# Kernel optimization log

Hardware: AMD Instinct MI355X
Metric: run time of the kernel (lower is better)

Reference implementation:

```python
import jax, jax.numpy as jnp
import numpy as np

B, T, TR, D, H = 8, 1024, 256, 1024, 16
HS = D // H  # head size = 64
FF = 4 * D


def _ln(x, g, b, eps=1e-5):
    m = jnp.mean(x, axis=-1, keepdims=True)
    v = jnp.mean((x - m) ** 2, axis=-1, keepdims=True)
    return (x - m) * jax.lax.rsqrt(v + eps) * g + b


def setup_inputs() -> dict:
    key = jax.random.key(0)
    ks = jax.random.split(key, 24)
    w = lambda i, shape: jax.random.normal(ks[i], shape, dtype=jnp.float32) * 0.02
    return {
        "x": jax.random.normal(ks[0], (B, T, D), dtype=jnp.float32),
        # reduced positional embedding table (gathered by arange == table itself)
        "pos_emb": w(1, (TR, D)),
        # inner standard Block params
        "blk_ln1_g": jnp.ones((D,), jnp.float32), "blk_ln1_b": jnp.zeros((D,), jnp.float32),
        "blk_wq": w(2, (H, D, HS)), "blk_wk": w(3, (H, D, HS)), "blk_wv": w(4, (H, D, HS)),
        "blk_wo": w(5, (D, D)), "blk_bo": jnp.zeros((D,), jnp.float32),
        "blk_ln2_g": jnp.ones((D,), jnp.float32), "blk_ln2_b": jnp.zeros((D,), jnp.float32),
        "blk_w1": w(6, (D, FF)), "blk_b1": jnp.zeros((FF,), jnp.float32),
        "blk_w2": w(7, (FF, D)), "blk_b2": jnp.zeros((D,), jnp.float32),
        # compressing cross-attention params
        "ln1_g": jnp.ones((D,), jnp.float32), "ln1_b": jnp.zeros((D,), jnp.float32),
        "ca_wq": w(8, (H, D, HS)), "ca_wk": w(9, (H, D, HS)), "ca_wv": w(10, (H, D, HS)),
        "ca_wo": w(11, (D, D)), "ca_bo": jnp.zeros((D,), jnp.float32),
        "ln2_g": jnp.ones((D,), jnp.float32), "ln2_b": jnp.zeros((D,), jnp.float32),
        "ff_w1": w(12, (D, FF)), "ff_b1": jnp.zeros((FF,), jnp.float32),
        "ff_w2": w(13, (FF, D)), "ff_b2": jnp.zeros((D,), jnp.float32),
    }


def reference(x, pos_emb, blk_ln1_g, blk_ln1_b, blk_wq, blk_wk, blk_wv, blk_wo, blk_bo,
              blk_ln2_g, blk_ln2_b, blk_w1, blk_b1, blk_w2, blk_b2,
              ln1_g, ln1_b, ca_wq, ca_wk, ca_wv, ca_wo, ca_bo,
              ln2_g, ln2_b, ff_w1, ff_b1, ff_w2, ff_b2):
    b, t, c = x.shape
    scale = c ** -0.5  # matches q @ k^T * c**-0.5 in source

    # ---- inner standard Block: y = x + sa(ln1(x)); y = y + ffwd(ln2(y)) ----
    h = _ln(x, blk_ln1_g, blk_ln1_b)
    q = jnp.einsum('btc,hcs->bhts', h, blk_wq)
    k = jnp.einsum('btc,hcs->bhts', h, blk_wk)
    v = jnp.einsum('btc,hcs->bhts', h, blk_wv)
    wei = jnp.einsum('bhts,bhus->bhtu', q, k) * scale
    causal = jnp.tril(jnp.ones((t, t), dtype=bool))
    wei = jax.nn.softmax(jnp.where(causal, wei, -jnp.inf), axis=-1)
    att = jnp.einsum('bhtu,bhus->bhts', wei, v)
    att = att.transpose(0, 2, 1, 3).reshape(b, t, c) @ blk_wo + blk_bo
    y = x + att
    h2 = _ln(y, blk_ln2_g, blk_ln2_b)
    y = y + (jax.nn.relu(h2 @ blk_w1 + blk_b1) @ blk_w2 + blk_b2)

    # outer residual in CompressingBlock.forward
    x = x + y

    # ---- compressing cross-attention: queries/values from x, keys from pos emb ----
    h1 = _ln(x, ln1_g, ln1_b)
    q = jnp.einsum('btc,hcs->bhts', h1, ca_wq)
    kk = jnp.einsum('rc,hcs->hrs', pos_emb, ca_wk)  # same for every batch
    v = jnp.einsum('btc,hcs->bhts', h1, ca_wv)
    wei = jnp.einsum('bhts,hrs->bhtr', q, kk) * scale  # [b,h,t,tr]
    tr = pos_emb.shape[0]
    mask = jnp.tril(jnp.ones((t, tr), dtype=bool))  # tril[:t,:tr]
    wei = jax.nn.softmax(jnp.where(mask, wei, -jnp.inf), axis=-1)
    # transpose then wei^T @ v -> compressed sequence length tr
    out = jnp.einsum('bhtr,bhts->bhrs', wei, v)
    out = out.transpose(0, 2, 1, 3).reshape(b, tr, c) @ ca_wo + ca_bo

    # ---- final FFN with residual ----
    h3 = _ln(out, ln2_g, ln2_b)
    out = out + (jax.nn.relu(h3 @ ff_w1 + ff_b1) @ ff_w2 + ff_b2)
    return out
```

## Files before the change

kernel.cpp:

```cpp
#include <hip/hip_runtime.h>
#include <stdint.h>

typedef unsigned short u16;
typedef __attribute__((ext_vector_type(8))) short short8;
typedef __attribute__((ext_vector_type(4))) float f32x4;

#define MFMA16(A,B,C) __builtin_amdgcn_mfma_f32_16x16x32_bf16(A,B,C,0,0,0)

static __device__ __forceinline__ u16 f2bf(float f) {
  union { float f; unsigned u; } v; v.f = f;
  unsigned r = v.u + 0x7FFFu + ((v.u >> 16) & 1u);
  return (u16)(r >> 16);
}

static __device__ __forceinline__ void gload16(const void* g, void* l) {
  __builtin_amdgcn_global_load_lds(
      (const __attribute__((address_space(1))) void*)(uintptr_t)g,
      (__attribute__((address_space(3))) void*)(uint32_t)(uintptr_t)l,
      16, 0, 0);
}

static __device__ __forceinline__ int xcd_swz() {
  const int gx = gridDim.x, gy = gridDim.y, nwg = gx * gy;
  const int orig = blockIdx.y * gx + blockIdx.x;
  const int q = nwg >> 3, rm = nwg & 7, xcd = orig & 7, idx = orig >> 3;
  return (xcd < rm ? xcd * (q + 1) : rm * (q + 1) + (xcd - rm) * q) + idx;
}

#define GPH(CUR, STAGE_STMT, TAIL_STMT) do { \
  short8 af_[4], bf_[4]; \
  _Pragma("unroll") \
  for (int mf = 0; mf < 4; ++mf) { \
    const int r = wm0 + mf * 16 + colL; \
    af_[mf] = *(const short8*)&lds[(CUR) + r * 32 + ((kgr ^ ((r >> 1) & 3)) << 3)]; \
  } \
  _Pragma("unroll") \
  for (int nf = 0; nf < 4; ++nf) { \
    const int r = wn0 + nf * 16 + colL; \
    bf_[nf] = *(const short8*)&lds[(CUR) + 4096 + r * 32 + ((kgr ^ ((r >> 1) & 3)) << 3)]; \
  } \
  STAGE_STMT; \
  _Pragma("unroll") \
  for (int mf = 0; mf < 4; ++mf) \
    _Pragma("unroll") \
    for (int nf = 0; nf < 4; ++nf) \
      acc[mf][nf] = MFMA16(af_[mf], bf_[nf], acc[mf][nf]); \
  TAIL_STMT; \
  __builtin_amdgcn_sched_barrier(0); \
  __builtin_amdgcn_s_barrier(); \
  asm volatile("" ::: "memory"); \
} while (0)

__global__ __launch_bounds__(256) void gemm128p(
    const u16* __restrict__ A, const u16* __restrict__ Wt,
    float* __restrict__ Cf, u16* __restrict__ Cb,
    const float* __restrict__ bias,
    const float* __restrict__ res1, const float* __restrict__ res2,
    int M, int N, int K, int relu)
{
  __shared__ u16 lds[24576];
  const int tid = threadIdx.x;
  const int wid = tid >> 6, lane = tid & 63;
  const int colL = lane & 15, kgr = lane >> 4;
  const int wm0 = (wid & 1) * 64, wn0 = (wid >> 1) * 64;
  const int w = xcd_swz();
  const int m0 = (w / gridDim.y) * 128, n0 = (w % gridDim.y) * 128;
  const int U = K >> 5;
  f32x4 acc[4][4] = {};

  auto stageP = [&](int u, int bufo) {
    const int kb = u * 32;
#pragma unroll
    for (int i = 0; i < 2; ++i) {
      const int c = i * 256 + tid;
      const int row = c >> 2, slot = c & 3;
      const int cs = kb + ((slot ^ ((row >> 1) & 3)) << 3);
      gload16(A  + (size_t)(m0 + row) * K + cs,
              &lds[bufo + ((i * 256 + wid * 64) << 3)]);
      gload16(Wt + (size_t)(n0 + row) * K + cs,
              &lds[bufo + 4096 + ((i * 256 + wid * 64) << 3)]);
    }
  };

  int c0 = 0, c1 = 8192, c2 = 16384;
  stageP(0, c0); stageP(1, c1);
  asm volatile("s_waitcnt vmcnt(4)" ::: "memory");
  __builtin_amdgcn_s_barrier();
  asm volatile("" ::: "memory");

  for (int u = 0; u < U; ++u) {
    GPH(c0,
        { if (u + 2 < U) stageP(u + 2, c2); },
        { if (u + 2 < U) { asm volatile("s_waitcnt vmcnt(4)" ::: "memory"); }
          else           { asm volatile("s_waitcnt vmcnt(0)" ::: "memory"); } });
    const int tmp = c0; c0 = c1; c1 = c2; c2 = tmp;
  }

#pragma unroll
  for (int mf = 0; mf < 4; ++mf) {
#pragma unroll
    for (int nf = 0; nf < 4; ++nf) {
      const int n = n0 + wn0 + nf * 16 + colL;
      const float bv = bias ? bias[n] : 0.f;
#pragma unroll
      for (int rr = 0; rr < 4; ++rr) {
        const int m = m0 + wm0 + mf * 16 + kgr * 4 + rr;
        const size_t off = (size_t)m * N + n;
        float v = acc[mf][nf][rr] + bv;
        if (res1) v += res1[off];
        if (res2) v += res2[off];
        if (relu) v = fmaxf(v, 0.f);
        if (Cf) Cf[off] = v; else Cb[off] = f2bf(v);
      }
    }
  }
}

__global__ __launch_bounds__(256) void gemm128ks(
    const u16* __restrict__ A, const u16* __restrict__ Wt,
    float* __restrict__ Pf, int lda, int N, int K)
{
  __shared__ u16 lds[24576];
  const int tid = threadIdx.x;
  const int wid = tid >> 6, lane = tid & 63;
  const int colL = lane & 15, kgr = lane >> 4;
  const int wm0 = (wid & 1) * 64, wn0 = (wid >> 1) * 64;
  const int w = xcd_swz();
  const int m0 = (w / gridDim.y) * 128, n0 = (w % gridDim.y) * 128;
  const int koff = blockIdx.z * K;
  const int U = K >> 5;
  f32x4 acc[4][4] = {};

  auto stageP = [&](int u, int bufo) {
    const int kb = koff + u * 32;
#pragma unroll
    for (int i = 0; i < 2; ++i) {
      const int c = i * 256 + tid;
      const int row = c >> 2, slot = c & 3;
      const int cs = kb + ((slot ^ ((row >> 1) & 3)) << 3);
      gload16(A  + (size_t)(m0 + row) * lda + cs,
              &lds[bufo + ((i * 256 + wid * 64) << 3)]);
      gload16(Wt + (size_t)(n0 + row) * lda + cs,
              &lds[bufo + 4096 + ((i * 256 + wid * 64) << 3)]);
    }
  };

  int c0 = 0, c1 = 8192, c2 = 16384;
  stageP(0, c0); stageP(1, c1);
  asm volatile("s_waitcnt vmcnt(4)" ::: "memory");
  __builtin_amdgcn_s_barrier();
  asm volatile("" ::: "memory");

  for (int u = 0; u < U; ++u) {
    GPH(c0,
        { if (u + 2 < U) stageP(u + 2, c2); },
        { if (u + 2 < U) { asm volatile("s_waitcnt vmcnt(4)" ::: "memory"); }
          else           { asm volatile("s_waitcnt vmcnt(0)" ::: "memory"); } });
    const int tmp = c0; c0 = c1; c1 = c2; c2 = tmp;
  }

  float* out = Pf + (size_t)blockIdx.z * gridDim.x * 128 * N;
#pragma unroll
  for (int mf = 0; mf < 4; ++mf)
#pragma unroll
    for (int nf = 0; nf < 4; ++nf) {
      const int n = n0 + wn0 + nf * 16 + colL;
#pragma unroll
      for (int rr = 0; rr < 4; ++rr) {
        const int m = m0 + wm0 + mf * 16 + kgr * 4 + rr;
        out[(size_t)m * N + n] = acc[mf][nf][rr];
      }
    }
}

__global__ __launch_bounds__(256) void ffn2_reduce(
    const float* __restrict__ pf, const float* __restrict__ bias,
    const float* __restrict__ res, float* __restrict__ out)
{
  const size_t i = ((size_t)blockIdx.x * 256 + threadIdx.x) * 4;
  const size_t STRIDE = (size_t)2048 * 1024;
  const int col = (int)(i & 1023);
  float4 a = *(const float4*)(pf + i);
  const float4 b = *(const float4*)(pf + STRIDE + i);
  const float4 c = *(const float4*)(pf + 2 * STRIDE + i);
  const float4 d = *(const float4*)(pf + 3 * STRIDE + i);
  const float4 bv = *(const float4*)(bias + col);
  const float4 rv = *(const float4*)(res + i);
  float4 o;
  o.x = a.x + b.x + c.x + d.x + bv.x + rv.x;
  o.y = a.y + b.y + c.y + d.y + bv.y + rv.y;
  o.z = a.z + b.z + c.z + d.z + bv.z + rv.z;
  o.w = a.w + b.w + c.w + d.w + bv.w + rv.w;
  *(float4*)(out + i) = o;
}

__global__ __launch_bounds__(256) void ln_rows(
    const float* __restrict__ x, const float* __restrict__ g,
    const float* __restrict__ bt, u16* __restrict__ out)
{
  const int row = blockIdx.x, tid = threadIdx.x;
  const float4 v = ((const float4*)(x + (size_t)row * 1024))[tid];
  float s  = v.x + v.y + v.z + v.w;
  float ss = v.x * v.x + v.y * v.y + v.z * v.z + v.w * v.w;
#pragma unroll
  for (int off = 32; off; off >>= 1) {
    s  += __shfl_xor(s, off);
    ss += __shfl_xor(ss, off);
  }
  __shared__ float red[8];
  const int wid = tid >> 6, lane = tid & 63;
  if (lane == 0) { red[wid] = s; red[4 + wid] = ss; }
  __syncthreads();
  s  = red[0] + red[1] + red[2] + red[3];
  ss = red[4] + red[5] + red[6] + red[7];
  const float mean = s * 0.0009765625f;
  const float var  = ss * 0.0009765625f - mean * mean;
  const float rstd = rsqrtf(var + 1e-5f);
  const float4 gg = ((const float4*)g)[tid];
  const float4 bb = ((const float4*)bt)[tid];
  uint2 ov;
  ov.x = (unsigned)f2bf((v.x - mean) * rstd * gg.x + bb.x) |
         ((unsigned)f2bf((v.y - mean) * rstd * gg.y + bb.y) << 16);
  ov.y = (unsigned)f2bf((v.z - mean) * rstd * gg.z + bb.z) |
         ((unsigned)f2bf((v.w - mean) * rstd * gg.w + bb.w) << 16);
  *(uint2*)(out + (size_t)row * 1024 + tid * 4) = ov;
}

__global__ __launch_bounds__(256) void transpose_w(
    const float* __restrict__ in, u16* __restrict__ out, int R, int C)
{
  __shared__ float t[32][33];
  const int c0 = blockIdx.x * 32, r0 = blockIdx.y * 32;
  const int tx = threadIdx.x & 31, ty = threadIdx.x >> 5;
#pragma unroll
  for (int i = 0; i < 32; i += 8)
    t[ty + i][tx] = in[(size_t)(r0 + ty + i) * C + c0 + tx];
  __syncthreads();
#pragma unroll
  for (int i = 0; i < 32; i += 8)
    out[(size_t)(c0 + ty + i) * R + r0 + tx] = f2bf(t[tx][ty + i]);
}

__global__ __launch_bounds__(256) void pack_head_w(
    const float* __restrict__ w, u16* __restrict__ out)
{
  __shared__ float t[32][33];
  const int h = blockIdx.z;
  const int s0 = blockIdx.x * 32, c0 = blockIdx.y * 32;
  const int tx = threadIdx.x & 31, ty = threadIdx.x >> 5;
#pragma unroll
  for (int i = 0; i < 32; i += 8)
    t[ty + i][tx] = w[((size_t)h * 1024 + c0 + ty + i) * 64 + s0 + tx];
  __syncthreads();
#pragma unroll
  for (int i = 0; i < 32; i += 8)
    out[((size_t)h * 64 + s0 + ty + i) * 1024 + c0 + tx] = f2bf(t[tx][ty + i]);
}

__global__ __launch_bounds__(256) void cvt_bf16(
    const float* __restrict__ in, u16* __restrict__ out)
{
  const int i = blockIdx.x * blockDim.x + threadIdx.x;
  const float4 v = ((const float4*)in)[i];
  uint2 ov;
  ov.x = (unsigned)f2bf(v.x) | ((unsigned)f2bf(v.y) << 16);
  ov.y = (unsigned)f2bf(v.z) | ((unsigned)f2bf(v.w) << 16);
  *(uint2*)(out + (size_t)i * 4) = ov;
}

__global__ __launch_bounds__(256) void vtrans(
    const u16* __restrict__ src, u16* __restrict__ dst, int coloff, int ld)
{
  __shared__ u16 tile[64][65];
  const int t0 = blockIdx.x * 64, h = blockIdx.y, b = blockIdx.z;
  const int lr = threadIdx.x >> 4;
  const int lc = (threadIdx.x & 15) * 4;
#pragma unroll
  for (int i = 0; i < 64; i += 16) {
    const u16* sp = src + (size_t)(b * 1024 + t0 + lr + i) * ld + coloff + h * 64 + lc;
    const uint2 v = *(const uint2*)sp;
    tile[lr + i][lc + 0] = (u16)(v.x & 0xffff);
    tile[lr + i][lc + 1] = (u16)(v.x >> 16);
    tile[lr + i][lc + 2] = (u16)(v.y & 0xffff);
    tile[lr + i][lc + 3] = (u16)(v.y >> 16);
  }
  __syncthreads();
#pragma unroll
  for (int i = 0; i < 64; i += 16) {
    const int s = lr + i;
    uint2 ov;
    ov.x = (unsigned)tile[lc + 0][s] | ((unsigned)tile[lc + 1][s] << 16);
    ov.y = (unsigned)tile[lc + 2][s] | ((unsigned)tile[lc + 3][s] << 16);
    *(uint2*)(dst + (size_t)((b * 16 + h) * 64 + s) * 1024 + t0 + lc) = ov;
  }
}

__global__ __launch_bounds__(512) void attn_inner(
    const u16* __restrict__ qkv, const u16* __restrict__ vt,
    u16* __restrict__ att)
{
  __shared__ u16 Kl[128 * 64];
  __shared__ u16 Vl[64 * 128];
  __shared__ u16 Pl[8 * 16 * 128];
  const int p = blockIdx.x, h = blockIdx.y, b = blockIdx.z;
  const int tid = threadIdx.x, wid = tid >> 6, lane = tid & 63;
  const int col = lane & 15, kgr = lane >> 4;
  const float scale = 0.03125f;
  u16* pw = &Pl[wid * 2048];

  auto run_q = [&](int tb) {
    short8 qf[2];
    {
      const int trow = tb * 128 + wid * 16 + col;
      const u16* qp = qkv + (size_t)(b * 1024 + trow) * 3072 + h * 64 + kgr * 8;
      qf[0] = *(const short8*)qp;
      qf[1] = *(const short8*)(qp + 32);
    }
    f32x4 o[4] = {};
    float lrun[4];
#pragma unroll
    for (int r = 0; r < 4; ++r) lrun[r] = 0.f;

    for (int kt = 0; kt <= tb * 128; kt += 128) {
#pragma unroll
      for (int i = 0; i < 2; ++i) {
        const int e = i * 4096 + tid * 8;
        const int rk = e >> 6, uk = (e >> 3) & 7;
        gload16(qkv + (size_t)(b * 1024 + kt + rk) * 3072 + 1024 + h * 64 +
                    ((uk ^ (rk & 7)) << 3),
                &Kl[i * 4096 + wid * 512]);
        const int rv = e >> 7, uv = (e >> 3) & 15;
        gload16(vt + (size_t)((b * 16 + h) * 64 + rv) * 1024 + kt +
                    ((uv ^ (rv & 7)) << 3),
                &Vl[i * 4096 + wid * 512]);
      }
      __syncthreads();
      f32x4 s[8];
      __builtin_amdgcn_s_setprio(1);
#pragma unroll
      for (int nt = 0; nt < 8; ++nt) {
        const int rk = nt * 16 + col;
        const short8 k0 = *(const short8*)&Kl[rk * 64 + ((kgr ^ (rk & 7)) << 3)];
        const short8 k1 = *(const short8*)&Kl[rk * 64 + (((kgr + 4) ^ (rk & 7)) << 3)];
        f32x4 a = {};
        a = MFMA16(qf[0], k0, a);
        a = MFMA16(qf[1], k1, a);
        s[nt] = a;
      }
      __builtin_amdgcn_s_setprio(0);
      float rs[4];
#pragma unroll
      for (int r = 0; r < 4; ++r) rs[r] = 0.f;
      const int tbase = tb * 128 + wid * 16 + kgr * 4;
      if (kt == tb * 128) {
#pragma unroll
        for (int nt = 0; nt < 8; ++nt) {
          const int kp = kt + nt * 16 + col;
#pragma unroll
          for (int r = 0; r < 4; ++r) {
            const float pv = (kp > tbase + r) ? 0.f : __expf(s[nt][r] * scale);
            s[nt][r] = pv;
            rs[r] += pv;
          }
        }
      } else {
#pragma unroll
        for (int nt = 0; nt < 8; ++nt)
#pragma unroll
          for (int r = 0; r < 4; ++r) {
            const float pv = __expf(s[nt][r] * scale);
            s[nt][r] = pv;
            rs[r] += pv;
          }
      }
#pragma unroll
      for (int r = 0; r < 4; ++r) {
#pragma unroll
        for (int off = 1; off < 16; off <<= 1)
          rs[r] += __shfl_xor(rs[r], off);
        lrun[r] += rs[r];
      }
#pragma unroll
      for (int nt = 0; nt < 8; ++nt)
#pragma unroll
        for (int r = 0; r < 4; ++r) {
          const int rp = kgr * 4 + r;
          pw[rp * 128 + ((nt * 16 + col) ^ ((rp & 7) << 3))] = f2bf(s[nt][r]);
        }
      __builtin_amdgcn_s_setprio(1);
#pragma unroll
      for (int ks = 0; ks < 4; ++ks) {
        const short8 pa = *(const short8*)&pw[col * 128 +
            ((ks * 32 + kgr * 8) ^ ((col & 7) << 3))];
#pragma unroll
        for (int st = 0; st < 4; ++st) {
          const int rv = st * 16 + col;
          const short8 vb = *(const short8*)&Vl[rv * 128 +
              (((ks * 4 + kgr) ^ (rv & 7)) << 3)];
          o[st] = MFMA16(pa, vb, o[st]);
        }
      }
      __builtin_amdgcn_s_setprio(0);
      __syncthreads();
    }
#pragma unroll
    for (int r = 0; r < 4; ++r) {
      const float inv = 1.f / lrun[r];
      const int t = tb * 128 + wid * 16 + kgr * 4 + r;
#pragma unroll
      for (int st = 0; st < 4; ++st)
        att[(size_t)(b * 1024 + t) * 1024 + h * 64 + st * 16 + col] =
            f2bf(o[st][r] * inv);
    }
  };

  run_q(7 - p);
  run_q(p);
}

__global__ __launch_bounds__(512) void attn_cross(
    const u16* __restrict__ qv, const u16* __restrict__ kk,
    const u16* __restrict__ vt, float* __restrict__ pout)
{
  __shared__ u16 KKl[256 * 64];
  __shared__ u16 Vl[64 * 128];
  __shared__ u16 PTl[256 * 128];
  const int h = blockIdx.x, b = blockIdx.y, ck = blockIdx.z;
  const int tid = threadIdx.x, wid = tid >> 6, lane = tid & 63;
  const int col = lane & 15, kgr = lane >> 4;
  const float scale = 0.03125f;
#pragma unroll
  for (int i = 0; i < 4; ++i) {
    const int e = i * 4096 + tid * 8;
    const int rk = e >> 6, uk = (e >> 3) & 7;
    gload16(kk + (size_t)rk * 1024 + h * 64 + ((uk ^ (rk & 7)) << 3),
            &KKl[i * 4096 + wid * 512]);
  }
  f32x4 oacc[2][4] = {};
  for (int tt = ck * 2; tt < ck * 2 + 2; ++tt) {
    const int t0 = tt * 128;
#pragma unroll
    for (int i = 0; i < 2; ++i) {
      const int e = i * 4096 + tid * 8;
      const int rv = e >> 7, uv = (e >> 3) & 15;
      gload16(vt + (size_t)((b * 16 + h) * 64 + rv) * 1024 + t0 +
                  ((uv ^ (rv & 7)) << 3),
              &Vl[i * 4096 + wid * 512]);
    }
    short8 qf0, qf1;
    {
      const int trow = t0 + wid * 16 + col;
      const u16* qp = qv + (size_t)(b * 1024 + trow) * 2048 + h * 64 + kgr * 8;
      qf0 = *(const short8*)qp;
      qf1 = *(const short8*)(qp + 32);
    }
    __syncthreads();
    f32x4 s[16];
#pragma unroll
    for (int rt = 0; rt < 16; ++rt) {
      const int rk = rt * 16 + col;
      const short8 k0 = *(const short8*)&KKl[rk * 64 + ((kgr ^ (rk & 7)) << 3)];
      const short8 k1 = *(const short8*)&KKl[rk * 64 + (((kgr + 4) ^ (rk & 7)) << 3)];
      f32x4 a = {};
      a = MFMA16(qf0, k0, a);
      a = MFMA16(qf1, k1, a);
      s[rt] = a;
    }
    float sm[4];
#pragma unroll
    for (int r = 0; r < 4; ++r) sm[r] = 0.f;
    const int tbase = t0 + wid * 16 + kgr * 4;
    if (t0 < 256) {
#pragma unroll
      for (int rt = 0; rt < 16; ++rt) {
        const int rp = rt * 16 + col;
#pragma unroll
        for (int r = 0; r < 4; ++r) {
          const float pv = (rp > tbase + r) ? 0.f : __expf(s[rt][r] * scale);
          s[rt][r] = pv;
          sm[r] += pv;
        }
      }
    } else {
#pragma unroll
      for (int rt = 0; rt < 16; ++rt)
#pragma unroll
        for (int r = 0; r < 4; ++r) {
          const float pv = __expf(s[rt][r] * scale);
          s[rt][r] = pv;
          sm[r] += pv;
        }
    }
#pragma unroll
    for (int r = 0; r < 4; ++r) {
#pragma unroll
      for (int off = 1; off < 16; off <<= 1)
        sm[r] += __shfl_xor(sm[r], off);
      sm[r] = 1.f / sm[r];
    }
#pragma unroll
    for (int rt = 0; rt < 16; ++rt)
#pragma unroll
      for (int r = 0; r < 4; ++r) {
        const int rpt = rt * 16 + col;
        PTl[rpt * 128 + ((wid * 16 + kgr * 4 + r) ^ ((rpt & 7) << 3))] =
            f2bf(s[rt][r] * sm[r]);
      }
    __syncthreads();
#pragma unroll
    for (int rr = 0; rr < 2; ++rr) {
      const int rb = (wid * 2 + rr) * 16;
#pragma unroll
      for (int ks = 0; ks < 4; ++ks) {
        const int rpt = rb + col;
        const short8 pa = *(const short8*)&PTl[rpt * 128 +
            ((ks * 32 + kgr * 8) ^ ((rpt & 7) << 3))];
#pragma unroll
        for (int st = 0; st < 4; ++st) {
          const int rv = st * 16 + col;
          const short8 vb = *(const short8*)&Vl[rv * 128 +
              (((ks * 4 + kgr) ^ (rv & 7)) << 3)];
          oacc[rr][st] = MFMA16(pa, vb, oacc[rr][st]);
        }
      }
    }
    __syncthreads();
  }
#pragma unroll
  for (int rr = 0; rr < 2; ++rr)
#pragma unroll
    for (int st = 0; st < 4; ++st)
#pragma unroll
      for (int r = 0; r < 4; ++r) {
        const int rpos = (wid * 2 + rr) * 16 + kgr * 4 + r;
        pout[(size_t)((ck * 8 + b) * 256 + rpos) * 1024 + h * 64 + st * 16 + col] =
            oacc[rr][st][r];
      }
}

__global__ __launch_bounds__(256) void cross_reduce(
    const float* __restrict__ pout, u16* __restrict__ outc)
{
  const size_t i = ((size_t)blockIdx.x * 256 + threadIdx.x) * 4;
  const size_t STRIDE = (size_t)8 * 256 * 1024;
  float4 a = *(const float4*)(pout + i);
  const float4 b = *(const float4*)(pout + STRIDE + i);
  const float4 c = *(const float4*)(pout + 2 * STRIDE + i);
  const float4 d = *(const float4*)(pout + 3 * STRIDE + i);
  a.x += b.x + c.x + d.x;
  a.y += b.y + c.y + d.y;
  a.z += b.z + c.z + d.z;
  a.w += b.w + c.w + d.w;
  uint2 ov;
  ov.x = (unsigned)f2bf(a.x) | ((unsigned)f2bf(a.y) << 16);
  ov.y = (unsigned)f2bf(a.z) | ((unsigned)f2bf(a.w) << 16);
  *(uint2*)(outc + i) = ov;
}

extern "C" void kernel_launch(void* const* d_in, const int* in_sizes, int n_in,
                              void* d_out, int out_size, void* d_ws, size_t ws_size,
                              hipStream_t stream)
{
  const float* x     = (const float*)d_in[0];
  const float* pos   = (const float*)d_in[1];
  const float* bln1g = (const float*)d_in[2];
  const float* bln1b = (const float*)d_in[3];
  const float* bwq   = (const float*)d_in[4];
  const float* bwk   = (const float*)d_in[5];
  const float* bwv   = (const float*)d_in[6];
  const float* bwo   = (const float*)d_in[7];
  const float* bbo   = (const float*)d_in[8];
  const float* bln2g = (const float*)d_in[9];
  const float* bln2b = (const float*)d_in[10];
  const float* bw1   = (const float*)d_in[11];
  const float* bb1   = (const float*)d_in[12];
  const float* bw2   = (const float*)d_in[13];
  const float* bb2   = (const float*)d_in[14];
  const float* ln1g  = (const float*)d_in[15];
  const float* ln1b  = (const float*)d_in[16];
  const float* cwq   = (const float*)d_in[17];
  const float* cwk   = (const float*)d_in[18];
  const float* cwv   = (const float*)d_in[19];
  const float* cwo   = (const float*)d_in[20];
  const float* cbo   = (const float*)d_in[21];
  const float* cln2g = (const float*)d_in[22];
  const float* cln2b = (const float*)d_in[23];
  const float* fw1   = (const float*)d_in[24];
  const float* fb1   = (const float*)d_in[25];
  const float* fw2   = (const float*)d_in[26];
  const float* fb2   = (const float*)d_in[27];

  char* ws = (char*)d_ws;
  size_t off = 0;
  auto alloc = [&](size_t bytes) -> void* {
    void* p = ws + off; off += (bytes + 255) & ~(size_t)255; return p;
  };
  u16* wqkv_t = (u16*)alloc((size_t)3072 * 1024 * 2);
  u16* wo_t   = (u16*)alloc((size_t)1024 * 1024 * 2);
  u16* w1_t   = (u16*)alloc((size_t)4096 * 1024 * 2);
  u16* w2_t   = (u16*)alloc((size_t)1024 * 4096 * 2);
  u16* cwqv_t = (u16*)alloc((size_t)2048 * 1024 * 2);
  u16* cwk_t  = (u16*)alloc((size_t)1024 * 1024 * 2);
  u16* cwo_t  = (u16*)alloc((size_t)1024 * 1024 * 2);
  u16* fw1_t  = (u16*)alloc((size_t)4096 * 1024 * 2);
  u16* fw2_t  = (u16*)alloc((size_t)1024 * 4096 * 2);
  u16* pos_bf = (u16*)alloc((size_t)256 * 1024 * 2);
  u16* kkb    = (u16*)alloc((size_t)256 * 1024 * 2);
  u16* act_ln = (u16*)alloc((size_t)8192 * 1024 * 2);
  u16* qkv    = (u16*)alloc((size_t)8192 * 3072 * 2);
  u16* att    = (u16*)alloc((size_t)8192 * 1024 * 2);
  u16* ffb    = (u16*)alloc((size_t)8192 * 4096 * 2);
  float* yb   = (float*)alloc((size_t)8192 * 1024 * 4);
  if (ws_size < off) return;
  float* x2    = (float*)qkv;
  u16*   qv    = qkv;
  u16*   vt    = ffb;
  u16*   outc  = att;
  float* zb    = yb;
  float* pacc  = yb;
  float* pacc2 = (float*)qkv;
  float* outp  = (float*)d_out;

  const dim3 B256(256), B512(512);
  pack_head_w<<<dim3(2, 32, 16), B256, 0, stream>>>(bwq, wqkv_t);
  pack_head_w<<<dim3(2, 32, 16), B256, 0, stream>>>(bwk, wqkv_t + 1024 * 1024);
  pack_head_w<<<dim3(2, 32, 16), B256, 0, stream>>>(bwv, wqkv_t + 2048 * 1024);
  transpose_w<<<dim3(32, 32),  B256, 0, stream>>>(bwo, wo_t, 1024, 1024);
  transpose_w<<<dim3(128, 32), B256, 0, stream>>>(bw1, w1_t, 1024, 4096);
  transpose_w<<<dim3(32, 128), B256, 0, stream>>>(bw2, w2_t, 4096, 1024);
  pack_head_w<<<dim3(2, 32, 16), B256, 0, stream>>>(cwq, cwqv_t);
  pack_head_w<<<dim3(2, 32, 16), B256, 0, stream>>>(cwv, cwqv_t + 1024 * 1024);
  pack_head_w<<<dim3(2, 32, 16), B256, 0, stream>>>(cwk, cwk_t);
  transpose_w<<<dim3(32, 32),  B256, 0, stream>>>(cwo, cwo_t, 1024, 1024);
  transpose_w<<<dim3(128, 32), B256, 0, stream>>>(fw1, fw1_t, 1024, 4096);
  transpose_w<<<dim3(32, 128), B256, 0, stream>>>(fw2, fw2_t, 4096, 1024);
  cvt_bf16<<<dim3(256), B256, 0, stream>>>(pos, pos_bf);

  ln_rows<<<dim3(8192), B256, 0, stream>>>(x, bln1g, bln1b, act_ln);
  gemm128p<<<dim3(64, 24), B256, 0, stream>>>(act_ln, wqkv_t, nullptr, qkv,
      nullptr, nullptr, nullptr, 8192, 3072, 1024, 0);
  vtrans<<<dim3(16, 16, 8), B256, 0, stream>>>(qkv, vt, 2048, 3072);
  attn_inner<<<dim3(4, 16, 8), B512, 0, stream>>>(qkv, vt, att);
  gemm128p<<<dim3(64, 8), B256, 0, stream>>>(att, wo_t, yb, nullptr,
      bbo, x, nullptr, 8192, 1024, 1024, 0);
  ln_rows<<<dim3(8192), B256, 0, stream>>>(yb, bln2g, bln2b, act_ln);
  gemm128p<<<dim3(64, 32), B256, 0, stream>>>(act_ln, w1_t, nullptr, ffb,
      bb1, nullptr, nullptr, 8192, 4096, 1024, 1);
  gemm128p<<<dim3(64, 8), B256, 0, stream>>>(ffb, w2_t, x2, nullptr,
      bb2, yb, x, 8192, 1024, 4096, 0);

  ln_rows<<<dim3(8192), B256, 0, stream>>>(x2, ln1g, ln1b, act_ln);
  gemm128p<<<dim3(64, 16), B256, 0, stream>>>(act_ln, cwqv_t, nullptr, qv,
      nullptr, nullptr, nullptr, 8192, 2048, 1024, 0);
  gemm128p<<<dim3(2, 8), B256, 0, stream>>>(pos_bf, cwk_t, nullptr, kkb,
      nullptr, nullptr, nullptr, 256, 1024, 1024, 0);
  vtrans<<<dim3(16, 16, 8), B256, 0, stream>>>(qv, vt, 1024, 2048);
  attn_cross<<<dim3(16, 8, 4), B512, 0, stream>>>(qv, kkb, vt, pacc);
  cross_reduce<<<dim3(2048), B256, 0, stream>>>(pacc, outc);
  gemm128p<<<dim3(16, 8), B256, 0, stream>>>(outc, cwo_t, zb, nullptr,
      cbo, nullptr, nullptr, 2048, 1024, 1024, 0);

  ln_rows<<<dim3(2048), B256, 0, stream>>>(zb, cln2g, cln2b, act_ln);
  gemm128p<<<dim3(16, 32), B256, 0, stream>>>(act_ln, fw1_t, nullptr, ffb,
      fb1, nullptr, nullptr, 2048, 4096, 1024, 1);
  gemm128ks<<<dim3(16, 8, 4), B256, 0, stream>>>(ffb, fw2_t, pacc2,
      4096, 1024, 1024);
  ffn2_reduce<<<dim3(2048), B256, 0, stream>>>(pacc2, fb2, zb, outp);
}
```

Before: 658.4 us.

## Split inner attention into one query tile per block with 64-wide key tiles

The causal inner attention kernel no longer pairs query tiles (7-p, p) inside one block. It launches one block per 128-row query tile, doubling the grid, and walks keys in 64-wide chunks instead of 128-wide ones, shrinking shared memory for K, V and P. This is meant to raise occupancy and parallelism and cut wasted masked work on the diagonal. The cost is lost load balancing across blocks, since late tiles take longer than early ones, plus more loop iterations and barriers per key.

```diff
diff --git a/kernel.cpp b/kernel.cpp
--- a/kernel.cpp
+++ b/kernel.cpp
@@ -299,123 +299,116 @@
     const u16* __restrict__ qkv, const u16* __restrict__ vt,
     u16* __restrict__ att)
 {
-  __shared__ u16 Kl[128 * 64];
-  __shared__ u16 Vl[64 * 128];
-  __shared__ u16 Pl[8 * 16 * 128];
-  const int p = blockIdx.x, h = blockIdx.y, b = blockIdx.z;
+  __shared__ u16 Kl[64 * 64];
+  __shared__ u16 Vl[64 * 64];
+  __shared__ u16 Pl[8 * 16 * 64];
+  const int tb = blockIdx.x, h = blockIdx.y, b = blockIdx.z;
   const int tid = threadIdx.x, wid = tid >> 6, lane = tid & 63;
   const int col = lane & 15, kgr = lane >> 4;
   const float scale = 0.03125f;
-  u16* pw = &Pl[wid * 2048];
-
-  auto run_q = [&](int tb) {
-    short8 qf[2];
+  u16* pw = &Pl[wid * 1024];
+
+  short8 qf[2];
+  {
+    const int trow = tb * 128 + wid * 16 + col;
+    const u16* qp = qkv + (size_t)(b * 1024 + trow) * 3072 + h * 64 + kgr * 8;
+    qf[0] = *(const short8*)qp;
+    qf[1] = *(const short8*)(qp + 32);
+  }
+  f32x4 o[4] = {};
+  float lrun[4];
+#pragma unroll
+  for (int r = 0; r < 4; ++r) lrun[r] = 0.f;
+
+  for (int kt = 0; kt <= tb * 128 + 64; kt += 64) {
     {
-      const int trow = tb * 128 + wid * 16 + col;
-      const u16* qp = qkv + (size_t)(b * 1024 + trow) * 3072 + h * 64 + kgr * 8;
-      qf[0] = *(const short8*)qp;
-      qf[1] = *(const short8*)(qp + 32);
-    }
-    f32x4 o[4] = {};
-    float lrun[4];
-#pragma unroll
-    for (int r = 0; r < 4; ++r) lrun[r] = 0.f;
-
-    for (int kt = 0; kt <= tb * 128; kt += 128) {
-#pragma unroll
-      for (int i = 0; i < 2; ++i) {
-        const int e = i * 4096 + tid * 8;
-        const int rk = e >> 6, uk = (e >> 3) & 7;
-        gload16(qkv + (size_t)(b * 1024 + kt + rk) * 3072 + 1024 + h * 64 +
-                    ((uk ^ (rk & 7)) << 3),
-                &Kl[i * 4096 + wid * 512]);
-        const int rv = e >> 7, uv = (e >> 3) & 15;
-        gload16(vt + (size_t)((b * 16 + h) * 64 + rv) * 1024 + kt +
-                    ((uv ^ (rv & 7)) << 3),
-                &Vl[i * 4096 + wid * 512]);
-      }
-      __syncthreads();
-      f32x4 s[8];
-      __builtin_amdgcn_s_setprio(1);
-#pragma unroll
-      for (int nt = 0; nt < 8; ++nt) {
-        const int rk = nt * 16 + col;
-        const short8 k0 = *(const short8*)&Kl[rk * 64 + ((kgr ^ (rk & 7)) << 3)];
-        const short8 k1 = *(const short8*)&Kl[rk * 64 + (((kgr + 4) ^ (rk & 7)) << 3)];
-        f32x4 a = {};
-        a = MFMA16(qf[0], k0, a);
-        a = MFMA16(qf[1], k1, a);
-        s[nt] = a;
-      }
-      __builtin_amdgcn_s_setprio(0);
-      float rs[4];
-#pragma unroll
-      for (int r = 0; r < 4; ++r) rs[r] = 0.f;
-      const int tbase = tb * 128 + wid * 16 + kgr * 4;
-      if (kt == tb * 128) {
-#pragma unroll
-        for (int nt = 0; nt < 8; ++nt) {
-          const int kp = kt + nt * 16 + col;
-#pragma unroll
-          for (int r = 0; r < 4; ++r) {
-            const float pv = (kp > tbase + r) ? 0.f : __expf(s[nt][r] * scale);
-            s[nt][r] = pv;
-            rs[r] += pv;
-          }
+      const int e = tid * 8;
+      const int rk = e >> 6, uk = (e >> 3) & 7;
+      gload16(qkv + (size_t)(b * 1024 + kt + rk) * 3072 + 1024 + h * 64 +
+                  ((uk ^ (rk & 7)) << 3),
+              &Kl[wid * 512]);
+      gload16(vt + (size_t)((b * 16 + h) * 64 + rk) * 1024 + kt +
+                  ((uk ^ (rk & 7)) << 3),
+              &Vl[wid * 512]);
+    }
+    __syncthreads();
+    f32x4 s[4];
+    __builtin_amdgcn_s_setprio(1);
+#pragma unroll
+    for (int nt = 0; nt < 4; ++nt) {
+      const int rka = nt * 16 + col;
+      const short8 k0 = *(const short8*)&Kl[rka * 64 + ((kgr ^ (rka & 7)) << 3)];
+      const short8 k1 = *(const short8*)&Kl[rka * 64 + (((kgr + 4) ^ (rka & 7)) << 3)];
+      f32x4 a = {};
+      a = MFMA16(qf[0], k0, a);
+      a = MFMA16(qf[1], k1, a);
+      s[nt] = a;
+    }
+    __builtin_amdgcn_s_setprio(0);
+    float rs[4];
+#pragma unroll
+    for (int r = 0; r < 4; ++r) rs[r] = 0.f;
+    const int tbase = tb * 128 + wid * 16 + kgr * 4;
+    if (kt >= tb * 128) {
+#pragma unroll
+      for (int nt = 0; nt < 4; ++nt) {
+        const int kp = kt + nt * 16 + col;
+#pragma unroll
+        for (int r = 0; r < 4; ++r) {
+          const float pv = (kp > tbase + r) ? 0.f : __expf(s[nt][r] * scale);
+          s[nt][r] = pv;
+          rs[r] += pv;
         }
-      } else {
-#pragma unroll
-        for (int nt = 0; nt < 8; ++nt)
-#pragma unroll
-          for (int r = 0; r < 4; ++r) {
-            const float pv = __expf(s[nt][r] * scale);
-            s[nt][r] = pv;
-            rs[r] += pv;
-          }
-      }
+      }
+    } else {
+#pragma unroll
+      for (int nt = 0; nt < 4; ++nt)
+#pragma unroll
+        for (int r = 0; r < 4; ++r) {
+          const float pv = __expf(s[nt][r] * scale);
+          s[nt][r] = pv;
+          rs[r] += pv;
+        }
+    }
+#pragma unroll
+    for (int r = 0; r < 4; ++r) {
+#pragma unroll
+      for (int off = 1; off < 16; off <<= 1)
+        rs[r] += __shfl_xor(rs[r], off);
+      lrun[r] += rs[r];
+    }
+#pragma unroll
+    for (int nt = 0; nt < 4; ++nt)
 #pragma unroll
       for (int r = 0; r < 4; ++r) {
-#pragma unroll
-        for (int off = 1; off < 16; off <<= 1)
-          rs[r] += __shfl_xor(rs[r], off);
-        lrun[r] += rs[r];
-      }
-#pragma unroll
-      for (int nt = 0; nt < 8; ++nt)
-#pragma unroll
-        for (int r = 0; r < 4; ++r) {
-          const int rp = kgr * 4 + r;
-          pw[rp * 128 + ((nt * 16 + col) ^ ((rp & 7) << 3))] = f2bf(s[nt][r]);
-        }
-      __builtin_amdgcn_s_setprio(1);
-#pragma unroll
-      for (int ks = 0; ks < 4; ++ks) {
-        const short8 pa = *(const short8*)&pw[col * 128 +
-            ((ks * 32 + kgr * 8) ^ ((col & 7) << 3))];
-#pragma unroll
-        for (int st = 0; st < 4; ++st) {
-          const int rv = st * 16 + col;
-          const short8 vb = *(const short8*)&Vl[rv * 128 +
-              (((ks * 4 + kgr) ^ (rv & 7)) << 3)];
-          o[st] = MFMA16(pa, vb, o[st]);
-        }
-      }
-      __builtin_amdgcn_s_setprio(0);
-      __syncthreads();
-    }
-#pragma unroll
-    for (int r = 0; r < 4; ++r) {
-      const float inv = 1.f / lrun[r];
-      const int t = tb * 128 + wid * 16 + kgr * 4 + r;
-#pragma unroll
-      for (int st = 0; st < 4; ++st)
-        att[(size_t)(b * 1024 + t) * 1024 + h * 64 + st * 16 + col] =
-            f2bf(o[st][r] * inv);
-    }
-  };
-
-  run_q(7 - p);
-  run_q(p);
+        const int rp = kgr * 4 + r;
+        pw[rp * 64 + ((nt * 16 + col) ^ ((rp & 7) << 3))] = f2bf(s[nt][r]);
+      }
+    __builtin_amdgcn_s_setprio(1);
+#pragma unroll
+    for (int ks = 0; ks < 2; ++ks) {
+      const short8 pa = *(const short8*)&pw[col * 64 +
+          ((ks * 32 + kgr * 8) ^ ((col & 7) << 3))];
+#pragma unroll
+      for (int st = 0; st < 4; ++st) {
+        const int rv = st * 16 + col;
+        const short8 vb = *(const short8*)&Vl[rv * 64 +
+            (((ks * 4 + kgr) ^ (rv & 7)) << 3)];
+        o[st] = MFMA16(pa, vb, o[st]);
+      }
+    }
+    __builtin_amdgcn_s_setprio(0);
+    __syncthreads();
+  }
+#pragma unroll
+  for (int r = 0; r < 4; ++r) {
+    const float inv = 1.f / lrun[r];
+    const int t = tb * 128 + wid * 16 + kgr * 4 + r;
+#pragma unroll
+    for (int st = 0; st < 4; ++st)
+      att[(size_t)(b * 1024 + t) * 1024 + h * 64 + st * 16 + col] =
+          f2bf(o[st][r] * inv);
+  }
 }
 
 __global__ __launch_bounds__(512) void attn_cross(
@@ -640,7 +633,7 @@
   gemm128p<<<dim3(64, 24), B256, 0, stream>>>(act_ln, wqkv_t, nullptr, qkv,
       nullptr, nullptr, nullptr, 8192, 3072, 1024, 0);
   vtrans<<<dim3(16, 16, 8), B256, 0, stream>>>(qkv, vt, 2048, 3072);
-  attn_inner<<<dim3(4, 16, 8), B512, 0, stream>>>(qkv, vt, att);
+  attn_inner<<<dim3(8, 16, 8), B512, 0, stream>>>(qkv, vt, att);
   gemm128p<<<dim3(64, 8), B256, 0, stream>>>(att, wo_t, yb, nullptr,
       bbo, x, nullptr, 8192, 1024, 1024, 0);
   ln_rows<<<dim3(8192), B256, 0, stream>>>(yb, bln2g, bln2b, act_ln);
```

Result: slower. 675.2 us (+2.5%).
